# Kernel tuning notes

Measured on AMD Instinct MI355X. Metric: run time of the kernel, lower is better.

## Reference

```python
import jax, jax.numpy as jnp
import numpy as np

DIM = 1024
NUM_HEADS = 16
HEAD_DIM = DIM // NUM_HEADS
SCALE = HEAD_DIM ** -0.5
EPS = 1e-5


def layernorm(x, gamma, beta):
    mu = jnp.mean(x, axis=-1, keepdims=True)
    var = jnp.mean(jnp.square(x - mu), axis=-1, keepdims=True)
    return (x - mu) * jax.lax.rsqrt(var + EPS) * gamma + beta


def setup_inputs() -> dict:
    key = jax.random.key(0)
    ks = jax.random.split(key, 12)
    B, Lq, Lk = 2, 2048, 2048
    s = 0.02
    return {
        "q": jax.random.normal(ks[0], (B, Lq, DIM), jnp.float32),
        "k": jax.random.normal(ks[1], (B, Lk, DIM), jnp.float32),
        "v": jax.random.normal(ks[2], (B, Lk, DIM), jnp.float32),
        "Wq": jax.random.normal(ks[3], (DIM, DIM), jnp.float32) * s,
        "Wk": jax.random.normal(ks[4], (DIM, DIM), jnp.float32) * s,
        "Wv": jax.random.normal(ks[5], (DIM, DIM), jnp.float32) * s,
        "gq": jnp.ones((HEAD_DIM,), jnp.float32),
        "bq": jnp.zeros((HEAD_DIM,), jnp.float32),
        "gk": jnp.ones((HEAD_DIM,), jnp.float32),
        "bk": jnp.zeros((HEAD_DIM,), jnp.float32),
        "Wo": jax.random.normal(ks[6], (DIM, DIM), jnp.float32) * s,
        "bo": jnp.zeros((DIM,), jnp.float32),
    }


def reference(q, k, v, Wq, Wk, Wv, gq, bq, gk, bk, Wo, bo):
    B, Lq, _ = q.shape
    Lk = k.shape[1]
    # projections: Linear(dim_in, dim) with no bias -> x @ W.T (W stored [out, in])
    qh = (q @ Wq.T).reshape(B, Lq, NUM_HEADS, HEAD_DIM).transpose(0, 2, 1, 3)
    kh = (k @ Wk.T).reshape(B, Lk, NUM_HEADS, HEAD_DIM).transpose(0, 2, 1, 3)
    vh = (v @ Wv.T).reshape(B, Lk, NUM_HEADS, HEAD_DIM).transpose(0, 2, 1, 3)
    # per-head LayerNorm on head_dim (QK-norm)
    qh = layernorm(qh, gq, bq) * SCALE
    kh = layernorm(kh, gk, bk)
    # sigmoid attention (no softmax, no row normalization)
    attn = jax.nn.sigmoid(jnp.einsum("bhqd,bhkd->bhqk", qh, kh))
    x = jnp.einsum("bhqk,bhkd->bhqd", attn, vh)
    x = x.transpose(0, 2, 1, 3).reshape(B, Lq, DIM)
    return x @ Wo.T + bo
```

## Files before the change

kernel.cpp:

```cpp
#include <hip/hip_runtime.h>
#include <stdint.h>

#define BATCH 2
#define SEQ   2048
#define DIM   1024
#define NH    16
#define MTOT  (BATCH*SEQ)
#define LN_EPS 1e-5f
#define Q_FOLD_SCALE (-0.1803368801111204f)

typedef __bf16 bf16x8 __attribute__((ext_vector_type(8)));
typedef float  f32x4  __attribute__((ext_vector_type(4)));

__device__ __forceinline__ unsigned short f2bf(float f) {
  uint32_t u = __float_as_uint(f);
  u += 0x7fffu + ((u >> 16) & 1u);
  return (unsigned short)(u >> 16);
}
__device__ __forceinline__ unsigned short f2bf_rh(float f) {
  uint32_t u = __float_as_uint(f) + 0x8000u;
  return (unsigned short)(u >> 16);
}

__device__ __forceinline__ void gload_lds16(const void* g, void* lds) {
  __builtin_amdgcn_global_load_lds(
      (const __attribute__((address_space(1))) uint32_t*)g,
      (__attribute__((address_space(3))) uint32_t*)lds, 16, 0, 0);
}

#define VMCNT(n) asm volatile("s_waitcnt vmcnt(" #n ")" ::: "memory")
#define BAR() do { __builtin_amdgcn_s_barrier(); __builtin_amdgcn_sched_barrier(0); } while (0)
#define DSFENCE() do {                                        \
    __builtin_amdgcn_sched_barrier(0);                        \
    asm volatile("s_waitcnt lgkmcnt(0)" ::: "memory");        \
    __builtin_amdgcn_sched_barrier(0);                        \
  } while (0)
#define ROT3(a, b, c) do { unsigned short* _t3 = (a); (a) = (b); (b) = (c); (c) = _t3; } while (0)
#define SWAP2(a, b) do { unsigned short* _t2 = (a); (a) = (b); (b) = _t2; } while (0)

__global__ void cvt_f32_bf16(const float* __restrict__ s0, unsigned short* __restrict__ d0,
                             const float* __restrict__ s1, unsigned short* __restrict__ d1,
                             const float* __restrict__ s2, unsigned short* __restrict__ d2,
                             const float* __restrict__ s3, unsigned short* __restrict__ d3,
                             int n) {
  int z = blockIdx.y;
  const float* s = z == 0 ? s0 : z == 1 ? s1 : z == 2 ? s2 : s3;
  unsigned short* d = z == 0 ? d0 : z == 1 ? d1 : z == 2 ? d2 : d3;
  if (s == nullptr) return;
  int i = (blockIdx.x * 256 + threadIdx.x) * 4;
  if (i >= n) return;
  float4 v = *(const float4*)(s + i);
  ushort4 o;
  o.x = f2bf(v.x); o.y = f2bf(v.y); o.z = f2bf(v.z); o.w = f2bf(v.w);
  *(ushort4*)(d + i) = o;
}

__global__ __launch_bounds__(256, 3)
void gemm_qkv(const unsigned short* __restrict__ Aq, const unsigned short* __restrict__ Ak,
              const unsigned short* __restrict__ Av,
              const unsigned short* __restrict__ Wqp, const unsigned short* __restrict__ Wkp,
              const unsigned short* __restrict__ Wvp,
              const float* __restrict__ gq, const float* __restrict__ bq,
              const float* __restrict__ gk, const float* __restrict__ bk,
              unsigned short* __restrict__ qh, unsigned short* __restrict__ kh,
              unsigned short* __restrict__ vT) {
  __shared__ unsigned short Asm[3][4096];
  __shared__ unsigned short Bsm[3][4096];
  const int z = blockIdx.z;
  const unsigned short* A = z == 0 ? Aq : z == 1 ? Ak : Av;
  const unsigned short* W = z == 0 ? Wqp : z == 1 ? Wkp : Wvp;
  const int t = threadIdx.x, w = t >> 6, l = t & 63, l15 = l & 15, lhi = l >> 4;
  const int wm = w >> 1, wn = w & 1;
  const int m0 = blockIdx.x * 128, n0 = blockIdx.y * 128;
  const int sr0 = t >> 2, sc = (t & 3) ^ (((t >> 2) >> 1) & 3);
  const int fsw = (l15 >> 1) & 3;

  unsigned short *ac = &Asm[0][0], *an = &Asm[1][0], *af_ = &Asm[2][0];
  unsigned short *bc = &Bsm[0][0], *bn = &Bsm[1][0], *bf_ = &Bsm[2][0];

  f32x4 acc[4][4] = {};

#define STAGE_G(ap, bp, kt) do {                                                  \
    int k0 = (kt) * 32;                                                           \
    gload_lds16(A + (size_t)(m0 + sr0) * 1024 + k0 + sc * 8, (ap) + t * 8);       \
    gload_lds16(A + (size_t)(m0 + 64 + sr0) * 1024 + k0 + sc * 8,                 \
                (ap) + (t + 256) * 8);                                            \
    gload_lds16(W + (size_t)(n0 + sr0) * 1024 + k0 + sc * 8, (bp) + t * 8);       \
    gload_lds16(W + (size_t)(n0 + 64 + sr0) * 1024 + k0 + sc * 8,                 \
                (bp) + (t + 256) * 8);                                            \
  } while (0)

  STAGE_G(ac, bc, 0);
  STAGE_G(an, bn, 1);
  for (int kt = 0; kt < 32; ++kt) {
    if (kt < 30)       { STAGE_G(af_, bf_, kt + 2); VMCNT(8); }
    else if (kt == 30) { VMCNT(4); }
    else               { VMCNT(0); }
    BAR();
    bf16x8 afr[4], bfr[4];
#pragma unroll
    for (int mi = 0; mi < 4; ++mi)
      afr[mi] = *(const bf16x8*)&ac[(wm * 64 + mi * 16 + l15) * 32 + ((lhi ^ fsw) * 8)];
#pragma unroll
    for (int ni = 0; ni < 4; ++ni)
      bfr[ni] = *(const bf16x8*)&bc[(wn * 64 + ni * 16 + l15) * 32 + ((lhi ^ fsw) * 8)];
    __builtin_amdgcn_s_setprio(1);
#pragma unroll
    for (int mi = 0; mi < 4; ++mi)
#pragma unroll
      for (int ni = 0; ni < 4; ++ni)
        acc[mi][ni] = __builtin_amdgcn_mfma_f32_16x16x32_bf16(afr[mi], bfr[ni], acc[mi][ni], 0, 0, 0);
    __builtin_amdgcn_s_setprio(0);
    BAR();
    ROT3(ac, an, af_);
    ROT3(bc, bn, bf_);
  }
#undef STAGE_G

  const int h = (n0 >> 6) + wn;
  if (z == 2) {
#pragma unroll
    for (int mi = 0; mi < 4; ++mi)
#pragma unroll
      for (int r = 0; r < 4; ++r) {
        int gm = m0 + wm * 64 + mi * 16 + lhi * 4 + r;
        int b = gm >> 11, pos = gm & 2047;
#pragma unroll
        for (int ni = 0; ni < 4; ++ni)
          vT[(((size_t)(b * NH + h)) * 64 + ni * 16 + l15) * SEQ + pos] = f2bf(acc[mi][ni][r]);
      }
  } else {
    const float* G  = z ? gk : gq;
    const float* Bt = z ? bk : bq;
    unsigned short* outp = z ? kh : qh;
    const float scl = z ? 1.f : Q_FOLD_SCALE;
    float g[4], bt[4];
#pragma unroll
    for (int ni = 0; ni < 4; ++ni) { g[ni] = G[ni * 16 + l15]; bt[ni] = Bt[ni * 16 + l15]; }
#pragma unroll
    for (int mi = 0; mi < 4; ++mi)
#pragma unroll
      for (int r = 0; r < 4; ++r) {
        float x[4], s = 0.f, s2 = 0.f;
#pragma unroll
        for (int ni = 0; ni < 4; ++ni) { x[ni] = acc[mi][ni][r]; s += x[ni]; s2 += x[ni] * x[ni]; }
#pragma unroll
        for (int msk = 1; msk < 16; msk <<= 1) {
          s  += __shfl_xor(s,  msk, 64);
          s2 += __shfl_xor(s2, msk, 64);
        }
        float mu = s * (1.f / 64.f);
        float var = s2 * (1.f / 64.f) - mu * mu;
        float rstd = rsqrtf(var + LN_EPS);
        int gm = m0 + wm * 64 + mi * 16 + lhi * 4 + r;
        int b = gm >> 11, pos = gm & 2047;
        size_t base = (((size_t)(b * NH + h)) * SEQ + pos) * 64;
#pragma unroll
        for (int ni = 0; ni < 4; ++ni) {
          float y = ((x[ni] - mu) * rstd * g[ni] + bt[ni]) * scl;
          outp[base + ni * 16 + l15] = f2bf(y);
        }
      }
  }
}

__global__ __launch_bounds__(256, 3)
void gemm_out(const unsigned short* __restrict__ A, const unsigned short* __restrict__ W,
              const float* __restrict__ bias, float* __restrict__ outf) {
  __shared__ unsigned short Asm[3][4096];
  __shared__ unsigned short Bsm[3][2048];
  const int t = threadIdx.x, w = t >> 6, l = t & 63, l15 = l & 15, lhi = l >> 4;
  const int wm = w >> 1, wn = w & 1;
  const int m0 = blockIdx.x * 128, n0 = blockIdx.y * 64;
  const int sr0 = t >> 2, sc = (t & 3) ^ (((t >> 2) >> 1) & 3);
  const int fsw = (l15 >> 1) & 3;

  unsigned short *ac = &Asm[0][0], *an = &Asm[1][0], *af_ = &Asm[2][0];
  unsigned short *bc = &Bsm[0][0], *bn = &Bsm[1][0], *bf_ = &Bsm[2][0];
  f32x4 acc[4][2] = {};

#define STAGE_G(ap, bp, kt) do {                                                  \
    int k0 = (kt) * 32;                                                           \
    gload_lds16(A + (size_t)(m0 + sr0) * 1024 + k0 + sc * 8, (ap) + t * 8);       \
    gload_lds16(A + (size_t)(m0 + 64 + sr0) * 1024 + k0 + sc * 8,                 \
                (ap) + (t + 256) * 8);                                            \
    gload_lds16(W + (size_t)(n0 + sr0) * 1024 + k0 + sc * 8, (bp) + t * 8);       \
  } while (0)

  STAGE_G(ac, bc, 0);
  STAGE_G(an, bn, 1);
  for (int kt = 0; kt < 32; ++kt) {
    if (kt < 30)       { STAGE_G(af_, bf_, kt + 2); VMCNT(6); }
    else if (kt == 30) { VMCNT(3); }
    else               { VMCNT(0); }
    BAR();
    bf16x8 afr[4], bfr[2];
#pragma unroll
    for (int mi = 0; mi < 4; ++mi)
      afr[mi] = *(const bf16x8*)&ac[(wm * 64 + mi * 16 + l15) * 32 + ((lhi ^ fsw) * 8)];
#pragma unroll
    for (int ni = 0; ni < 2; ++ni)
      bfr[ni] = *(const bf16x8*)&bc[(wn * 32 + ni * 16 + l15) * 32 + ((lhi ^ fsw) * 8)];
    __builtin_amdgcn_s_setprio(1);
#pragma unroll
    for (int mi = 0; mi < 4; ++mi)
#pragma unroll
      for (int ni = 0; ni < 2; ++ni)
        acc[mi][ni] = __builtin_amdgcn_mfma_f32_16x16x32_bf16(afr[mi], bfr[ni], acc[mi][ni], 0, 0, 0);
    __builtin_amdgcn_s_setprio(0);
    BAR();
    ROT3(ac, an, af_);
    ROT3(bc, bn, bf_);
  }
#undef STAGE_G
  float bb[2];
#pragma unroll
  for (int ni = 0; ni < 2; ++ni) bb[ni] = bias[n0 + wn * 32 + ni * 16 + l15];
#pragma unroll
  for (int mi = 0; mi < 4; ++mi)
#pragma unroll
    for (int r = 0; r < 4; ++r) {
      int gm = m0 + wm * 64 + mi * 16 + lhi * 4 + r;
      float* op = outf + (size_t)gm * 1024 + n0 + wn * 32 + l15;
#pragma unroll
      for (int ni = 0; ni < 2; ++ni) op[ni * 16] = acc[mi][ni][r] + bb[ni];
    }
}

__global__ __launch_bounds__(1024, 4)
void attn_kernel(const unsigned short* __restrict__ qh,
                 const unsigned short* __restrict__ kh,
                 const unsigned short* __restrict__ vT,
                 unsigned short* __restrict__ x) {
  __shared__ unsigned short SMEM[69632];
  const int t = threadIdx.x, w = t >> 6, l = t & 63, l15 = l & 15, lhi = l >> 4;
  const int g = w >> 3, wq = w & 7;
  const int L = blockIdx.x;
  const int xcd = L & 7, j = L >> 3;
  const int bh = xcd * 4 + (j >> 3);
  const int qt = j & 7;
  const int b = bh >> 4;
  const unsigned short* Q = qh + (size_t)bh * SEQ * 64;
  const unsigned short* K = kh + (size_t)bh * SEQ * 64;
  const unsigned short* V = vT + (size_t)bh * 64 * SEQ;
  unsigned short* Pw = &SMEM[32768 + w * 2304];
  const int qbase = qt * 256 + wq * 32;

  bf16x8 qf[2][2];
#pragma unroll
  for (int mi = 0; mi < 2; ++mi)
#pragma unroll
    for (int kb = 0; kb < 2; ++kb)
      qf[mi][kb] = *(const bf16x8*)&Q[(size_t)(qbase + mi * 16 + l15) * 64 + kb * 32 + lhi * 8];

  f32x4 o[2][4] = {};
  const int p = t >> 9, tid = t & 511, r0 = tid >> 3, c0 = tid & 7;

  unsigned short *kcur = &SMEM[0],     *knxt = &SMEM[8192];
  unsigned short *vcur = &SMEM[16384], *vnxt = &SMEM[24576];

#define STAGE_PAIR(kb_, vb_, sp) do {                                                  \
    int kv0_ = (2 * (sp) + p) * 64;                                                    \
    gload_lds16(K + (size_t)(kv0_ + r0) * 64 + (c0 ^ (r0 & 7)) * 8,                    \
                (kb_) + p * 4096 + tid * 8);                                           \
    gload_lds16(V + (size_t)r0 * SEQ + kv0_ + (c0 ^ (r0 & 7)) * 8,                     \
                (vb_) + p * 4096 + tid * 8);                                           \
  } while (0)

  STAGE_PAIR(kcur, vcur, 0);
  for (int s = 0; s < 16; ++s) {
    if (s < 15) { STAGE_PAIR(knxt, vnxt, s + 1); VMCNT(2); }
    else        { VMCNT(0); }
    BAR();

    const unsigned short* kc = kcur + g * 4096;
    const unsigned short* vc = vcur + g * 4096;

    f32x4 sS[2][4] = {};
    __builtin_amdgcn_s_setprio(1);
#pragma unroll
    for (int ni = 0; ni < 4; ++ni)
#pragma unroll
      for (int kb = 0; kb < 2; ++kb) {
        bf16x8 kfr = *(const bf16x8*)&kc[(ni * 16 + l15) * 64 + (((kb * 4 + lhi) ^ (l15 & 7)) * 8)];
        sS[0][ni] = __builtin_amdgcn_mfma_f32_16x16x32_bf16(qf[0][kb], kfr, sS[0][ni], 0, 0, 0);
        sS[1][ni] = __builtin_amdgcn_mfma_f32_16x16x32_bf16(qf[1][kb], kfr, sS[1][ni], 0, 0, 0);
      }
    __builtin_amdgcn_s_setprio(0);

#pragma unroll
    for (int mi = 0; mi < 2; ++mi)
#pragma unroll
      for (int ni = 0; ni < 4; ++ni)
#pragma unroll
        for (int r = 0; r < 4; ++r) {
          float pv = __builtin_amdgcn_rcpf(1.0f + __builtin_amdgcn_exp2f(sS[mi][ni][r]));
          Pw[(mi * 16 + lhi * 4 + r) * 72 + ni * 16 + l15] = f2bf_rh(pv);
        }
    DSFENCE();

    __builtin_amdgcn_s_setprio(1);
#pragma unroll
    for (int kq = 0; kq < 2; ++kq) {
      bf16x8 pf0 = *(const bf16x8*)&Pw[l15 * 72 + kq * 32 + lhi * 8];
      bf16x8 pf1 = *(const bf16x8*)&Pw[(16 + l15) * 72 + kq * 32 + lhi * 8];
#pragma unroll
      for (int di = 0; di < 4; ++di) {
        bf16x8 vfr = *(const bf16x8*)&vc[(di * 16 + l15) * 64 + (((kq * 4 + lhi) ^ (l15 & 7)) * 8)];
        o[0][di] = __builtin_amdgcn_mfma_f32_16x16x32_bf16(pf0, vfr, o[0][di], 0, 0, 0);
        o[1][di] = __builtin_amdgcn_mfma_f32_16x16x32_bf16(pf1, vfr, o[1][di], 0, 0, 0);
      }
    }
    __builtin_amdgcn_s_setprio(0);
    BAR();

    SWAP2(kcur, knxt);
    SWAP2(vcur, vnxt);
  }
#undef STAGE_PAIR

  float* Ob = (float*)SMEM;
  if (g == 1) {
#pragma unroll
    for (int mi = 0; mi < 2; ++mi)
#pragma unroll
      for (int di = 0; di < 4; ++di)
        *(f32x4*)&Ob[wq * 2048 + (mi * 4 + di) * 256 + l * 4] = o[mi][di];
  }
  DSFENCE();
  BAR();
  if (g == 0) {
#pragma unroll
    for (int mi = 0; mi < 2; ++mi)
#pragma unroll
      for (int di = 0; di < 4; ++di) {
        f32x4 op = *(const f32x4*)&Ob[wq * 2048 + (mi * 4 + di) * 256 + l * 4];
#pragma unroll
        for (int r = 0; r < 4; ++r) o[mi][di][r] += op[r];
      }
#pragma unroll
    for (int mi = 0; mi < 2; ++mi)
#pragma unroll
      for (int r = 0; r < 4; ++r) {
        int pos = qbase + mi * 16 + lhi * 4 + r;
        size_t base = ((size_t)b * SEQ + pos) * DIM + (bh & 15) * 64;
#pragma unroll
        for (int di = 0; di < 4; ++di)
          x[base + di * 16 + l15] = f2bf(o[mi][di][r]);
      }
  }
}

extern "C" void kernel_launch(void* const* d_in, const int* in_sizes, int n_in,
                              void* d_out, int out_size, void* d_ws, size_t ws_size,
                              hipStream_t stream) {
  (void)in_sizes; (void)n_in; (void)out_size; (void)ws_size;
  const float* q  = (const float*)d_in[0];
  const float* k  = (const float*)d_in[1];
  const float* v  = (const float*)d_in[2];
  const float* Wq = (const float*)d_in[3];
  const float* Wk = (const float*)d_in[4];
  const float* Wv = (const float*)d_in[5];
  const float* gq = (const float*)d_in[6];
  const float* bq = (const float*)d_in[7];
  const float* gk = (const float*)d_in[8];
  const float* bk = (const float*)d_in[9];
  const float* Wo = (const float*)d_in[10];
  const float* bo = (const float*)d_in[11];
  float* out = (float*)d_out;

  char* ws = (char*)d_ws;
  const size_t MB = 1ull << 20;
  unsigned short* qb  = (unsigned short*)(ws + 0);
  unsigned short* kb  = (unsigned short*)(ws + 8  * MB);
  unsigned short* vb  = (unsigned short*)(ws + 16 * MB);
  unsigned short* Wqb = (unsigned short*)(ws + 24 * MB);
  unsigned short* Wkb = (unsigned short*)(ws + 26 * MB);
  unsigned short* Wvb = (unsigned short*)(ws + 28 * MB);
  unsigned short* Wob = (unsigned short*)(ws + 30 * MB);
  unsigned short* qhb = (unsigned short*)(ws + 32 * MB);
  unsigned short* khb = (unsigned short*)(ws + 40 * MB);
  unsigned short* vTb = (unsigned short*)(ws + 48 * MB);
  unsigned short* xb  = qb;

  const int nIn = MTOT * DIM;
  const int nW  = DIM * DIM;

  cvt_f32_bf16<<<dim3(nIn / 1024, 3), 256, 0, stream>>>(q, qb, k, kb, v, vb, nullptr, nullptr, nIn);
  cvt_f32_bf16<<<dim3(nW / 1024, 4), 256, 0, stream>>>(Wq, Wqb, Wk, Wkb, Wv, Wvb, Wo, Wob, nW);

  gemm_qkv<<<dim3(MTOT / 128, DIM / 128, 3), 256, 0, stream>>>(qb, kb, vb, Wqb, Wkb, Wvb,
                                                               gq, bq, gk, bk, qhb, khb, vTb);

  attn_kernel<<<dim3(256), 1024, 0, stream>>>(qhb, khb, vTb, xb);

  gemm_out<<<dim3(MTOT / 128, DIM / 64), 256, 0, stream>>>(xb, Wob, bo, out);
}
```

Baseline: 126.0 us.

## Shrink QKV GEMM tile to 64x128 with double buffering and merge conversion launches

```diff
diff --git a/kernel.cpp b/kernel.cpp
--- a/kernel.cpp
+++ b/kernel.cpp
@@ -35,18 +35,25 @@
     asm volatile("s_waitcnt lgkmcnt(0)" ::: "memory");        \
     __builtin_amdgcn_sched_barrier(0);                        \
   } while (0)
-#define ROT3(a, b, c) do { unsigned short* _t3 = (a); (a) = (b); (b) = (c); (c) = _t3; } while (0)
 #define SWAP2(a, b) do { unsigned short* _t2 = (a); (a) = (b); (b) = _t2; } while (0)
 
-__global__ void cvt_f32_bf16(const float* __restrict__ s0, unsigned short* __restrict__ d0,
-                             const float* __restrict__ s1, unsigned short* __restrict__ d1,
-                             const float* __restrict__ s2, unsigned short* __restrict__ d2,
-                             const float* __restrict__ s3, unsigned short* __restrict__ d3,
-                             int n) {
+__global__ void cvt_f32_bf16_all(const float* __restrict__ s0, unsigned short* __restrict__ d0,
+                                 const float* __restrict__ s1, unsigned short* __restrict__ d1,
+                                 const float* __restrict__ s2, unsigned short* __restrict__ d2,
+                                 const float* __restrict__ s3, unsigned short* __restrict__ d3,
+                                 const float* __restrict__ s4, unsigned short* __restrict__ d4,
+                                 const float* __restrict__ s5, unsigned short* __restrict__ d5,
+                                 const float* __restrict__ s6, unsigned short* __restrict__ d6,
+                                 int nIn, int nW) {
   int z = blockIdx.y;
-  const float* s = z == 0 ? s0 : z == 1 ? s1 : z == 2 ? s2 : s3;
-  unsigned short* d = z == 0 ? d0 : z == 1 ? d1 : z == 2 ? d2 : d3;
-  if (s == nullptr) return;
+  const float* s; unsigned short* d; int n;
+  if      (z == 0) { s = s0; d = d0; n = nIn; }
+  else if (z == 1) { s = s1; d = d1; n = nIn; }
+  else if (z == 2) { s = s2; d = d2; n = nIn; }
+  else if (z == 3) { s = s3; d = d3; n = nW; }
+  else if (z == 4) { s = s4; d = d4; n = nW; }
+  else if (z == 5) { s = s5; d = d5; n = nW; }
+  else             { s = s6; d = d6; n = nW; }
   int i = (blockIdx.x * 256 + threadIdx.x) * 4;
   if (i >= n) return;
   float4 v = *(const float4*)(s + i);
@@ -55,7 +62,7 @@
   *(ushort4*)(d + i) = o;
 }
 
-__global__ __launch_bounds__(256, 3)
+__global__ __launch_bounds__(256, 6)
 void gemm_qkv(const unsigned short* __restrict__ Aq, const unsigned short* __restrict__ Ak,
               const unsigned short* __restrict__ Av,
               const unsigned short* __restrict__ Wqp, const unsigned short* __restrict__ Wkp,
@@ -64,66 +71,62 @@
               const float* __restrict__ gk, const float* __restrict__ bk,
               unsigned short* __restrict__ qh, unsigned short* __restrict__ kh,
               unsigned short* __restrict__ vT) {
-  __shared__ unsigned short Asm[3][4096];
-  __shared__ unsigned short Bsm[3][4096];
+  __shared__ unsigned short Asm[2][2048];
+  __shared__ unsigned short Bsm[2][4096];
   const int z = blockIdx.z;
   const unsigned short* A = z == 0 ? Aq : z == 1 ? Ak : Av;
   const unsigned short* W = z == 0 ? Wqp : z == 1 ? Wkp : Wvp;
   const int t = threadIdx.x, w = t >> 6, l = t & 63, l15 = l & 15, lhi = l >> 4;
   const int wm = w >> 1, wn = w & 1;
-  const int m0 = blockIdx.x * 128, n0 = blockIdx.y * 128;
+  const int m0 = blockIdx.x * 64, n0 = blockIdx.y * 128;
   const int sr0 = t >> 2, sc = (t & 3) ^ (((t >> 2) >> 1) & 3);
   const int fsw = (l15 >> 1) & 3;
 
-  unsigned short *ac = &Asm[0][0], *an = &Asm[1][0], *af_ = &Asm[2][0];
-  unsigned short *bc = &Bsm[0][0], *bn = &Bsm[1][0], *bf_ = &Bsm[2][0];
-
-  f32x4 acc[4][4] = {};
+  unsigned short *ac = &Asm[0][0], *an = &Asm[1][0];
+  unsigned short *bc = &Bsm[0][0], *bn = &Bsm[1][0];
+
+  f32x4 acc[2][4] = {};
 
 #define STAGE_G(ap, bp, kt) do {                                                  \
     int k0 = (kt) * 32;                                                           \
     gload_lds16(A + (size_t)(m0 + sr0) * 1024 + k0 + sc * 8, (ap) + t * 8);       \
-    gload_lds16(A + (size_t)(m0 + 64 + sr0) * 1024 + k0 + sc * 8,                 \
-                (ap) + (t + 256) * 8);                                            \
     gload_lds16(W + (size_t)(n0 + sr0) * 1024 + k0 + sc * 8, (bp) + t * 8);       \
     gload_lds16(W + (size_t)(n0 + 64 + sr0) * 1024 + k0 + sc * 8,                 \
                 (bp) + (t + 256) * 8);                                            \
   } while (0)
 
   STAGE_G(ac, bc, 0);
-  STAGE_G(an, bn, 1);
   for (int kt = 0; kt < 32; ++kt) {
-    if (kt < 30)       { STAGE_G(af_, bf_, kt + 2); VMCNT(8); }
-    else if (kt == 30) { VMCNT(4); }
-    else               { VMCNT(0); }
-    BAR();
-    bf16x8 afr[4], bfr[4];
-#pragma unroll
-    for (int mi = 0; mi < 4; ++mi)
-      afr[mi] = *(const bf16x8*)&ac[(wm * 64 + mi * 16 + l15) * 32 + ((lhi ^ fsw) * 8)];
+    if (kt < 31) { STAGE_G(an, bn, kt + 1); VMCNT(3); }
+    else         { VMCNT(0); }
+    BAR();
+    bf16x8 afr[2], bfr[4];
+#pragma unroll
+    for (int mi = 0; mi < 2; ++mi)
+      afr[mi] = *(const bf16x8*)&ac[(wm * 32 + mi * 16 + l15) * 32 + ((lhi ^ fsw) * 8)];
 #pragma unroll
     for (int ni = 0; ni < 4; ++ni)
       bfr[ni] = *(const bf16x8*)&bc[(wn * 64 + ni * 16 + l15) * 32 + ((lhi ^ fsw) * 8)];
     __builtin_amdgcn_s_setprio(1);
 #pragma unroll
-    for (int mi = 0; mi < 4; ++mi)
+    for (int mi = 0; mi < 2; ++mi)
 #pragma unroll
       for (int ni = 0; ni < 4; ++ni)
         acc[mi][ni] = __builtin_amdgcn_mfma_f32_16x16x32_bf16(afr[mi], bfr[ni], acc[mi][ni], 0, 0, 0);
     __builtin_amdgcn_s_setprio(0);
     BAR();
-    ROT3(ac, an, af_);
-    ROT3(bc, bn, bf_);
+    SWAP2(ac, an);
+    SWAP2(bc, bn);
   }
 #undef STAGE_G
 
   const int h = (n0 >> 6) + wn;
   if (z == 2) {
 #pragma unroll
-    for (int mi = 0; mi < 4; ++mi)
+    for (int mi = 0; mi < 2; ++mi)
 #pragma unroll
       for (int r = 0; r < 4; ++r) {
-        int gm = m0 + wm * 64 + mi * 16 + lhi * 4 + r;
+        int gm = m0 + wm * 32 + mi * 16 + lhi * 4 + r;
         int b = gm >> 11, pos = gm & 2047;
 #pragma unroll
         for (int ni = 0; ni < 4; ++ni)
@@ -138,7 +141,7 @@
 #pragma unroll
     for (int ni = 0; ni < 4; ++ni) { g[ni] = G[ni * 16 + l15]; bt[ni] = Bt[ni * 16 + l15]; }
 #pragma unroll
-    for (int mi = 0; mi < 4; ++mi)
+    for (int mi = 0; mi < 2; ++mi)
 #pragma unroll
       for (int r = 0; r < 4; ++r) {
         float x[4], s = 0.f, s2 = 0.f;
@@ -152,7 +155,7 @@
         float mu = s * (1.f / 64.f);
         float var = s2 * (1.f / 64.f) - mu * mu;
         float rstd = rsqrtf(var + LN_EPS);
-        int gm = m0 + wm * 64 + mi * 16 + lhi * 4 + r;
+        int gm = m0 + wm * 32 + mi * 16 + lhi * 4 + r;
         int b = gm >> 11, pos = gm & 2047;
         size_t base = (((size_t)(b * NH + h)) * SEQ + pos) * 64;
 #pragma unroll
@@ -164,6 +167,7 @@
   }
 }
 
+#define ROT3(a, b, c) do { unsigned short* _t3 = (a); (a) = (b); (b) = (c); (c) = _t3; } while (0)
 __global__ __launch_bounds__(256, 3)
 void gemm_out(const unsigned short* __restrict__ A, const unsigned short* __restrict__ W,
               const float* __restrict__ bias, float* __restrict__ outf) {
@@ -386,11 +390,11 @@
   const int nIn = MTOT * DIM;
   const int nW  = DIM * DIM;
 
-  cvt_f32_bf16<<<dim3(nIn / 1024, 3), 256, 0, stream>>>(q, qb, k, kb, v, vb, nullptr, nullptr, nIn);
-  cvt_f32_bf16<<<dim3(nW / 1024, 4), 256, 0, stream>>>(Wq, Wqb, Wk, Wkb, Wv, Wvb, Wo, Wob, nW);
-
-  gemm_qkv<<<dim3(MTOT / 128, DIM / 128, 3), 256, 0, stream>>>(qb, kb, vb, Wqb, Wkb, Wvb,
-                                                               gq, bq, gk, bk, qhb, khb, vTb);
+  cvt_f32_bf16_all<<<dim3(nIn / 1024, 7), 256, 0, stream>>>(
+      q, qb, k, kb, v, vb, Wq, Wqb, Wk, Wkb, Wv, Wvb, Wo, Wob, nIn, nW);
+
+  gemm_qkv<<<dim3(MTOT / 64, DIM / 128, 3), 256, 0, stream>>>(qb, kb, vb, Wqb, Wkb, Wvb,
+                                                              gq, bq, gk, bk, qhb, khb, vTb);
 
   attn_kernel<<<dim3(256), 1024, 0, stream>>>(qhb, khb, vTb, xb);
 
```

Measured after the change: 134.5 us. 1.07x slower.

## Fuse fp32-to-bf16 activation conversion into QKV projection GEMM loads

Applied to the files above, without the earlier changes.

```diff
diff --git a/kernel.cpp b/kernel.cpp
--- a/kernel.cpp
+++ b/kernel.cpp
@@ -30,6 +30,11 @@
 
 #define VMCNT(n) asm volatile("s_waitcnt vmcnt(" #n ")" ::: "memory")
 #define BAR() do { __builtin_amdgcn_s_barrier(); __builtin_amdgcn_sched_barrier(0); } while (0)
+#define BARW() do {                                           \
+    asm volatile("s_waitcnt lgkmcnt(0)" ::: "memory");        \
+    __builtin_amdgcn_s_barrier();                             \
+    __builtin_amdgcn_sched_barrier(0);                        \
+  } while (0)
 #define DSFENCE() do {                                        \
     __builtin_amdgcn_sched_barrier(0);                        \
     asm volatile("s_waitcnt lgkmcnt(0)" ::: "memory");        \
@@ -38,15 +43,14 @@
 #define ROT3(a, b, c) do { unsigned short* _t3 = (a); (a) = (b); (b) = (c); (c) = _t3; } while (0)
 #define SWAP2(a, b) do { unsigned short* _t2 = (a); (a) = (b); (b) = _t2; } while (0)
 
-__global__ void cvt_f32_bf16(const float* __restrict__ s0, unsigned short* __restrict__ d0,
-                             const float* __restrict__ s1, unsigned short* __restrict__ d1,
-                             const float* __restrict__ s2, unsigned short* __restrict__ d2,
-                             const float* __restrict__ s3, unsigned short* __restrict__ d3,
-                             int n) {
+__global__ void cvt_w_bf16(const float* __restrict__ s0, unsigned short* __restrict__ d0,
+                           const float* __restrict__ s1, unsigned short* __restrict__ d1,
+                           const float* __restrict__ s2, unsigned short* __restrict__ d2,
+                           const float* __restrict__ s3, unsigned short* __restrict__ d3,
+                           int n) {
   int z = blockIdx.y;
   const float* s = z == 0 ? s0 : z == 1 ? s1 : z == 2 ? s2 : s3;
   unsigned short* d = z == 0 ? d0 : z == 1 ? d1 : z == 2 ? d2 : d3;
-  if (s == nullptr) return;
   int i = (blockIdx.x * 256 + threadIdx.x) * 4;
   if (i >= n) return;
   float4 v = *(const float4*)(s + i);
@@ -56,8 +60,8 @@
 }
 
 __global__ __launch_bounds__(256, 3)
-void gemm_qkv(const unsigned short* __restrict__ Aq, const unsigned short* __restrict__ Ak,
-              const unsigned short* __restrict__ Av,
+void gemm_qkv(const float* __restrict__ Aq, const float* __restrict__ Ak,
+              const float* __restrict__ Av,
               const unsigned short* __restrict__ Wqp, const unsigned short* __restrict__ Wkp,
               const unsigned short* __restrict__ Wvp,
               const float* __restrict__ gq, const float* __restrict__ bq,
@@ -67,7 +71,7 @@
   __shared__ unsigned short Asm[3][4096];
   __shared__ unsigned short Bsm[3][4096];
   const int z = blockIdx.z;
-  const unsigned short* A = z == 0 ? Aq : z == 1 ? Ak : Av;
+  const float* A = z == 0 ? Aq : z == 1 ? Ak : Av;
   const unsigned short* W = z == 0 ? Wqp : z == 1 ? Wkp : Wvp;
   const int t = threadIdx.x, w = t >> 6, l = t & 63, l15 = l & 15, lhi = l >> 4;
   const int wm = w >> 1, wn = w & 1;
@@ -75,47 +79,81 @@
   const int sr0 = t >> 2, sc = (t & 3) ^ (((t >> 2) >> 1) & 3);
   const int fsw = (l15 >> 1) & 3;
 
+  int aoffG[4], aoffL[4];
+#pragma unroll
+  for (int j = 0; j < 4; ++j) {
+    int i = t + 256 * j, row = i >> 3, c4 = i & 7;
+    aoffG[j] = row * 1024 + c4 * 4;
+    aoffL[j] = row * 32 + (((c4 >> 1) ^ ((row >> 1) & 3)) * 8) + (c4 & 1) * 4;
+  }
+
   unsigned short *ac = &Asm[0][0], *an = &Asm[1][0], *af_ = &Asm[2][0];
   unsigned short *bc = &Bsm[0][0], *bn = &Bsm[1][0], *bf_ = &Bsm[2][0];
 
   f32x4 acc[4][4] = {};
-
-#define STAGE_G(ap, bp, kt) do {                                                  \
+  float4 ra[4], rb[4];
+
+#define LOADA(R, kt) do {                                                         \
+    _Pragma("unroll")                                                             \
+    for (int j = 0; j < 4; ++j)                                                   \
+      R[j] = *(const float4*)(A + (size_t)m0 * 1024 + aoffG[j] + (kt) * 32);      \
+  } while (0)
+#define CVTA(R, sp) do {                                                          \
+    _Pragma("unroll")                                                             \
+    for (int j = 0; j < 4; ++j) {                                                 \
+      ushort4 h;                                                                  \
+      h.x = f2bf(R[j].x); h.y = f2bf(R[j].y);                                     \
+      h.z = f2bf(R[j].z); h.w = f2bf(R[j].w);                                     \
+      *(ushort4*)&(sp)[aoffL[j]] = h;                                             \
+    }                                                                             \
+  } while (0)
+#define STAGE_W(bp, kt) do {                                                      \
     int k0 = (kt) * 32;                                                           \
-    gload_lds16(A + (size_t)(m0 + sr0) * 1024 + k0 + sc * 8, (ap) + t * 8);       \
-    gload_lds16(A + (size_t)(m0 + 64 + sr0) * 1024 + k0 + sc * 8,                 \
-                (ap) + (t + 256) * 8);                                            \
     gload_lds16(W + (size_t)(n0 + sr0) * 1024 + k0 + sc * 8, (bp) + t * 8);       \
     gload_lds16(W + (size_t)(n0 + 64 + sr0) * 1024 + k0 + sc * 8,                 \
                 (bp) + (t + 256) * 8);                                            \
   } while (0)
-
-  STAGE_G(ac, bc, 0);
-  STAGE_G(an, bn, 1);
-  for (int kt = 0; kt < 32; ++kt) {
-    if (kt < 30)       { STAGE_G(af_, bf_, kt + 2); VMCNT(8); }
-    else if (kt == 30) { VMCNT(4); }
-    else               { VMCNT(0); }
-    BAR();
-    bf16x8 afr[4], bfr[4];
-#pragma unroll
-    for (int mi = 0; mi < 4; ++mi)
-      afr[mi] = *(const bf16x8*)&ac[(wm * 64 + mi * 16 + l15) * 32 + ((lhi ^ fsw) * 8)];
-#pragma unroll
-    for (int ni = 0; ni < 4; ++ni)
-      bfr[ni] = *(const bf16x8*)&bc[(wn * 64 + ni * 16 + l15) * 32 + ((lhi ^ fsw) * 8)];
-    __builtin_amdgcn_s_setprio(1);
-#pragma unroll
-    for (int mi = 0; mi < 4; ++mi)
-#pragma unroll
-      for (int ni = 0; ni < 4; ++ni)
-        acc[mi][ni] = __builtin_amdgcn_mfma_f32_16x16x32_bf16(afr[mi], bfr[ni], acc[mi][ni], 0, 0, 0);
-    __builtin_amdgcn_s_setprio(0);
-    BAR();
-    ROT3(ac, an, af_);
-    ROT3(bc, bn, bf_);
-  }
-#undef STAGE_G
+#define COMPUTE() do {                                                            \
+    bf16x8 afr[4], bfr[4];                                                        \
+    _Pragma("unroll")                                                             \
+    for (int mi = 0; mi < 4; ++mi)                                                \
+      afr[mi] = *(const bf16x8*)&ac[(wm * 64 + mi * 16 + l15) * 32 + ((lhi ^ fsw) * 8)]; \
+    _Pragma("unroll")                                                             \
+    for (int ni = 0; ni < 4; ++ni)                                                \
+      bfr[ni] = *(const bf16x8*)&bc[(wn * 64 + ni * 16 + l15) * 32 + ((lhi ^ fsw) * 8)]; \
+    __builtin_amdgcn_s_setprio(1);                                                \
+    _Pragma("unroll")                                                             \
+    for (int mi = 0; mi < 4; ++mi)                                                \
+      _Pragma("unroll")                                                           \
+      for (int ni = 0; ni < 4; ++ni)                                              \
+        acc[mi][ni] = __builtin_amdgcn_mfma_f32_16x16x32_bf16(afr[mi], bfr[ni], acc[mi][ni], 0, 0, 0); \
+    __builtin_amdgcn_s_setprio(0);                                                \
+  } while (0)
+#define STEP(kt, RL, RC) do {                                                     \
+    if ((kt) < 30) { LOADA(RL, (kt) + 2); STAGE_W(bf_, (kt) + 2); VMCNT(6); }     \
+    else           { VMCNT(0); }                                                  \
+    BARW();                                                                       \
+    if ((kt) < 31) CVTA(RC, an);                                                  \
+    COMPUTE();                                                                    \
+    BARW();                                                                       \
+    ROT3(ac, an, af_);                                                            \
+    ROT3(bc, bn, bf_);                                                            \
+  } while (0)
+
+  LOADA(ra, 0); STAGE_W(bc, 0);
+  LOADA(rb, 1); STAGE_W(bn, 1);
+  VMCNT(6);
+  CVTA(ra, ac);
+
+  for (int kt2 = 0; kt2 < 16; ++kt2) {
+    STEP(2 * kt2,     ra, rb);
+    STEP(2 * kt2 + 1, rb, ra);
+  }
+#undef STEP
+#undef COMPUTE
+#undef STAGE_W
+#undef CVTA
+#undef LOADA
 
   const int h = (n0 >> 6) + wn;
   if (z == 2) {
@@ -371,9 +409,7 @@
 
   char* ws = (char*)d_ws;
   const size_t MB = 1ull << 20;
-  unsigned short* qb  = (unsigned short*)(ws + 0);
-  unsigned short* kb  = (unsigned short*)(ws + 8  * MB);
-  unsigned short* vb  = (unsigned short*)(ws + 16 * MB);
+  unsigned short* xb  = (unsigned short*)(ws + 0);
   unsigned short* Wqb = (unsigned short*)(ws + 24 * MB);
   unsigned short* Wkb = (unsigned short*)(ws + 26 * MB);
   unsigned short* Wvb = (unsigned short*)(ws + 28 * MB);
@@ -381,15 +417,12 @@
   unsigned short* qhb = (unsigned short*)(ws + 32 * MB);
   unsigned short* khb = (unsigned short*)(ws + 40 * MB);
   unsigned short* vTb = (unsigned short*)(ws + 48 * MB);
-  unsigned short* xb  = qb;
-
-  const int nIn = MTOT * DIM;
-  const int nW  = DIM * DIM;
-
-  cvt_f32_bf16<<<dim3(nIn / 1024, 3), 256, 0, stream>>>(q, qb, k, kb, v, vb, nullptr, nullptr, nIn);
-  cvt_f32_bf16<<<dim3(nW / 1024, 4), 256, 0, stream>>>(Wq, Wqb, Wk, Wkb, Wv, Wvb, Wo, Wob, nW);
-
-  gemm_qkv<<<dim3(MTOT / 128, DIM / 128, 3), 256, 0, stream>>>(qb, kb, vb, Wqb, Wkb, Wvb,
+
+  const int nW = DIM * DIM;
+
+  cvt_w_bf16<<<dim3(nW / 1024, 4), 256, 0, stream>>>(Wq, Wqb, Wk, Wkb, Wv, Wvb, Wo, Wob, nW);
+
+  gemm_qkv<<<dim3(MTOT / 128, DIM / 128, 3), 256, 0, stream>>>(q, k, v, Wqb, Wkb, Wvb,
                                                                gq, bq, gk, bk, qhb, khb, vTb);
 
   attn_kernel<<<dim3(256), 1024, 0, stream>>>(qhb, khb, vTb, xb);
```

After: 121.3 us, median of 3. -3.7%, faster.
